# Kernel optimization log

Hardware: AMD Instinct MI355X
Metric: run time of the kernel (lower is better)

The kernel has to match this reference:

```python
import jax, jax.numpy as jnp
import numpy as np

NUM_EXPERTS = 8
IN_FEATURES = 2048
OUT_FEATURES = 5632
GROUP_SIZE = 64
NUM_TOKENS = 4096


def setup_inputs() -> dict:
    key = jax.random.key(0)
    k1, k2, k3, k4 = jax.random.split(key, 4)
    inp = jax.random.normal(k1, (NUM_TOKENS, IN_FEATURES), dtype=jnp.float32)
    # tokens are pre-sorted contiguously per expert; balanced routing
    tokens_per_expert = jnp.full((NUM_EXPERTS,), NUM_TOKENS // NUM_EXPERTS, dtype=jnp.int32)
    # int4 quantized weights stored as integer codes in [0, 16)
    weights = jax.random.randint(k2, (NUM_EXPERTS, IN_FEATURES, OUT_FEATURES), 0, 16, dtype=jnp.int32)
    n_groups = IN_FEATURES // GROUP_SIZE
    scales = jax.random.uniform(k3, (NUM_EXPERTS, n_groups, OUT_FEATURES, 1), dtype=jnp.float32,
                                minval=0.005, maxval=0.02)
    zeros = jax.random.normal(k4, (NUM_EXPERTS, n_groups, OUT_FEATURES, 1), dtype=jnp.float32) * 0.01
    scales_and_zeros = jnp.concatenate([scales, zeros], axis=-1)  # [E, K//G, N, 2]
    return {"input": inp, "tokens_per_expert": tokens_per_expert,
            "weights": weights, "scales_and_zeros": scales_and_zeros}


def _dequant(weights, scales_and_zeros):
    # torchao int4 convention: w = (q - 8) * scale + zero, grouped along K
    E, K, N = weights.shape
    n_groups = scales_and_zeros.shape[1]
    g = K // n_groups
    q = weights.astype(jnp.float32).reshape(E, n_groups, g, N)
    s = scales_and_zeros[..., 0][:, :, None, :]  # [E, K//G, 1, N]
    z = scales_and_zeros[..., 1][:, :, None, :]
    return ((q - 8.0) * s + z).reshape(E, K, N)


def reference(input, tokens_per_expert, weights, scales_and_zeros):
    num_tokens, K = input.shape
    E = weights.shape[0]
    W = _dequant(weights, scales_and_zeros)  # [E, K, N] float32
    # expert id of each (contiguous-sorted) token from cumsum boundaries
    cum = jnp.cumsum(tokens_per_expert)                      # [E]
    seg = jnp.searchsorted(cum, jnp.arange(num_tokens), side='right')  # [T]
    start = jnp.concatenate([jnp.zeros((1,), cum.dtype), cum[:-1]])
    pos = jnp.arange(num_tokens) - start[seg]                # slot within expert block
    # capacity-based grouped GEMM (balanced routing in setup: C = T // E)
    C = num_tokens // E
    buf = jnp.zeros((E, C, K), input.dtype).at[seg, pos].set(input)
    y = jnp.einsum('eck,ekn->ecn', buf, W)                   # per-expert GEMM
    return y[seg, pos]                                       # [T, N]
```

## Files before the change

kernel.cpp:

```cpp
#include <hip/hip_runtime.h>

#define NE    8
#define KDIM  2048
#define NDIM  5632
#define NTOK  4096
#define CAP   512
#define NGRP  32
#define BM    128
#define BN    128
#define BK    32
#define MT    4
#define NT    44
#define LDSS  40

#define K8      (KDIM / 8)
#define NBLK_N  (NDIM / 256)
#define PACK_BLOCKS (NE * K8 * NBLK_N)
#define ACV_BLOCKS  (NTOK * KDIM / (8 * 256))
#define PACKED_BYTES ((size_t)NE * K8 * NDIM * 4)
#define ABF_BYTES    ((size_t)NTOK * KDIM * 2)

typedef __attribute__((ext_vector_type(8))) short bf16x8;
typedef __attribute__((ext_vector_type(4))) short bf16x4;
typedef __attribute__((ext_vector_type(4))) float f32x4;

static __device__ __forceinline__ short f2bf(float f) {
    union { float f; unsigned u; } x; x.f = f;
    unsigned r = (x.u + 0x7fffu + ((x.u >> 16) & 1u)) >> 16;
    return (short)r;
}

__global__ __launch_bounds__(256)
void pack_kernel(const int* __restrict__ wq, const float* __restrict__ inp,
                 unsigned* __restrict__ pw, unsigned short* __restrict__ abf)
{
    const int bid = blockIdx.x;
    if (bid < PACK_BLOCKS) {
        const int e  = bid / (K8 * NBLK_N);
        const int r  = bid % (K8 * NBLK_N);
        const int k8 = r / NBLK_N;
        const int nb = r % NBLK_N;
        const int n  = nb * 256 + threadIdx.x;
        const int* src = wq + ((size_t)e * KDIM + k8 * 8) * NDIM + n;
        unsigned v = 0;
        #pragma unroll
        for (int j = 0; j < 8; ++j)
            v |= (unsigned)(src[(size_t)j * NDIM] & 15) << (4 * j);
        pw[((size_t)e * K8 + k8) * NDIM + n] = v;
    } else {
        const size_t t = (size_t)(bid - PACK_BLOCKS) * 256 + threadIdx.x;
        const float4* p = (const float4*)inp + t * 2;
        const float4 v0 = p[0], v1 = p[1];
        bf16x8 h;
        h[0] = f2bf(v0.x); h[1] = f2bf(v0.y); h[2] = f2bf(v0.z); h[3] = f2bf(v0.w);
        h[4] = f2bf(v1.x); h[5] = f2bf(v1.y); h[6] = f2bf(v1.z); h[7] = f2bf(v1.w);
        *((bf16x8*)abf + t) = h;
    }
}

__global__ __launch_bounds__(256, 2)
void hqq_gemm2(const unsigned short* __restrict__ abf,
               const unsigned*       __restrict__ pw,
               const float*          __restrict__ sz,
               float*                __restrict__ out)
{
    const int bid = blockIdx.x;
    const int e   = bid / (MT * NT);
    const int rem = bid % (MT * NT);
    const int nt  = rem >> 2;
    const int mt  = rem & 3;

    __shared__ __align__(16) short Alds[BM * LDSS];
    __shared__ __align__(16) short Blds[BN * LDSS];

    const int tid = threadIdx.x;
    const int m0  = e * CAP + mt * BM;
    const int n0  = nt * BN;

    const int a_kq  = tid & 3;
    const int a_row = tid >> 2;
    const int b_n   = tid & 127;
    const int b_h   = tid >> 7;

    const unsigned short* Ab = abf + (size_t)m0 * KDIM;
    const unsigned*       Wb = pw  + (size_t)e * K8 * NDIM + n0 + b_n;
    const float*          SZb = sz + (size_t)e * NGRP * (NDIM * 2) + (size_t)(n0 + b_n) * 2;

    f32x4 acc[4][4];
    #pragma unroll
    for (int i = 0; i < 4; ++i)
        #pragma unroll
        for (int j = 0; j < 4; ++j)
            acc[i][j] = (f32x4){0.f, 0.f, 0.f, 0.f};

    const int wave = tid >> 6;
    const int lane = tid & 63;
    const int wm = (wave >> 1) << 6;
    const int wn = (wave & 1) << 6;
    const int lr = lane & 15;
    const int lq = lane >> 4;

    for (int k0 = 0; k0 < KDIM; k0 += BK) {
        const int g = k0 >> 6;

        #pragma unroll
        for (int p = 0; p < 2; ++p) {
            const int row = a_row + p * 64;
            const bf16x8 v = *(const bf16x8*)(Ab + (size_t)row * KDIM + k0 + a_kq * 8);
            *(bf16x8*)&Alds[row * LDSS + a_kq * 8] = v;
        }

        const float2 s2 = *(const float2*)(SZb + (size_t)g * (NDIM * 2));
        const float s  = s2.x;
        const float z8 = s2.y - 8.f * s2.x;
        const unsigned* wp = Wb + ((size_t)(k0 >> 3) + b_h * 2) * NDIM;
        const unsigned u0 = wp[0];
        const unsigned u1 = wp[NDIM];
        bf16x8 bb0, bb1;
        #pragma unroll
        for (int j = 0; j < 8; ++j) {
            bb0[j] = f2bf(fmaf((float)((u0 >> (4 * j)) & 15u), s, z8));
            bb1[j] = f2bf(fmaf((float)((u1 >> (4 * j)) & 15u), s, z8));
        }
        *(bf16x8*)&Blds[b_n * LDSS + b_h * 16]     = bb0;
        *(bf16x8*)&Blds[b_n * LDSS + b_h * 16 + 8] = bb1;

        __syncthreads();

        bf16x8 af[4], bfv[4];
        #pragma unroll
        for (int i = 0; i < 4; ++i)
            af[i] = *(const bf16x8*)&Alds[(wm + i * 16 + lr) * LDSS + lq * 8];
        #pragma unroll
        for (int j = 0; j < 4; ++j)
            bfv[j] = *(const bf16x8*)&Blds[(wn + j * 16 + lr) * LDSS + lq * 8];
        #pragma unroll
        for (int i = 0; i < 4; ++i)
            #pragma unroll
            for (int j = 0; j < 4; ++j)
                acc[i][j] = __builtin_amdgcn_mfma_f32_16x16x32_bf16(af[i], bfv[j], acc[i][j], 0, 0, 0);

        __syncthreads();
    }

    const int orow0 = m0 + wm + lq * 4;
    const int ocol0 = n0 + wn + lr;
    #pragma unroll
    for (int i = 0; i < 4; ++i)
        #pragma unroll
        for (int r = 0; r < 4; ++r) {
            float* op = out + (size_t)(orow0 + i * 16 + r) * NDIM + ocol0;
            #pragma unroll
            for (int j = 0; j < 4; ++j)
                op[j * 16] = acc[i][j][r];
        }
}

__global__ __launch_bounds__(256, 2)
void hqq_gemm_fallback(const float* __restrict__ inp,
                       const int*   __restrict__ wq,
                       const float* __restrict__ sz,
                       float*       __restrict__ out)
{
    const int bid = blockIdx.x;
    const int e   = bid / (MT * NT);
    const int rem = bid % (MT * NT);
    const int nt  = rem >> 2;
    const int mt  = rem & 3;

    __shared__ __align__(16) short Alds[BM * LDSS];
    __shared__ __align__(16) short Blds[BN * LDSS];

    const int tid = threadIdx.x;
    const int m0  = e * CAP + mt * BM;
    const int n0  = nt * BN;

    const int a_kq  = tid & 7;
    const int a_row = tid >> 3;
    const int b_n   = tid & 127;
    const int b_h   = tid >> 7;

    const float* Ab  = inp + (size_t)m0 * KDIM;
    const int*   Wb  = wq  + (size_t)e * KDIM * NDIM + n0 + b_n;
    const float* SZb = sz  + (size_t)e * NGRP * (NDIM * 2) + (size_t)(n0 + b_n) * 2;

    f32x4 acc[4][4];
    #pragma unroll
    for (int i = 0; i < 4; ++i)
        #pragma unroll
        for (int j = 0; j < 4; ++j)
            acc[i][j] = (f32x4){0.f, 0.f, 0.f, 0.f};

    const int wave = tid >> 6;
    const int lane = tid & 63;
    const int wm = (wave >> 1) << 6;
    const int wn = (wave & 1) << 6;
    const int lr = lane & 15;
    const int lq = lane >> 4;

    for (int k0 = 0; k0 < KDIM; k0 += BK) {
        const int g = k0 >> 6;
        #pragma unroll
        for (int p = 0; p < 4; ++p) {
            const int row = a_row + p * 32;
            const float4 v = *(const float4*)(Ab + (size_t)row * KDIM + k0 + a_kq * 4);
            bf16x4 h;
            h[0] = f2bf(v.x); h[1] = f2bf(v.y); h[2] = f2bf(v.z); h[3] = f2bf(v.w);
            *(bf16x4*)&Alds[row * LDSS + a_kq * 4] = h;
        }
        const float2 s2 = *(const float2*)(SZb + (size_t)g * (NDIM * 2));
        const float s  = s2.x;
        const float z8 = s2.y - 8.f * s2.x;
        #pragma unroll
        for (int oo = 0; oo < 2; ++oo) {
            const int ko = b_h * 8 + oo * 16;
            const int* wp = Wb + (size_t)(k0 + ko) * NDIM;
            bf16x8 bb;
            #pragma unroll
            for (int j = 0; j < 8; ++j) {
                const float q = (float)wp[(size_t)j * NDIM];
                bb[j] = f2bf(fmaf(q, s, z8));
            }
            *(bf16x8*)&Blds[b_n * LDSS + ko] = bb;
        }
        __syncthreads();
        bf16x8 af[4], bfv[4];
        #pragma unroll
        for (int i = 0; i < 4; ++i)
            af[i] = *(const bf16x8*)&Alds[(wm + i * 16 + lr) * LDSS + lq * 8];
        #pragma unroll
        for (int j = 0; j < 4; ++j)
            bfv[j] = *(const bf16x8*)&Blds[(wn + j * 16 + lr) * LDSS + lq * 8];
        #pragma unroll
        for (int i = 0; i < 4; ++i)
            #pragma unroll
            for (int j = 0; j < 4; ++j)
                acc[i][j] = __builtin_amdgcn_mfma_f32_16x16x32_bf16(af[i], bfv[j], acc[i][j], 0, 0, 0);
        __syncthreads();
    }

    const int orow0 = m0 + wm + lq * 4;
    const int ocol0 = n0 + wn + lr;
    #pragma unroll
    for (int i = 0; i < 4; ++i)
        #pragma unroll
        for (int r = 0; r < 4; ++r) {
            float* op = out + (size_t)(orow0 + i * 16 + r) * NDIM + ocol0;
            #pragma unroll
            for (int j = 0; j < 4; ++j)
                op[j * 16] = acc[i][j][r];
        }
}

extern "C" void kernel_launch(void* const* d_in, const int* in_sizes, int n_in,
                              void* d_out, int out_size, void* d_ws, size_t ws_size,
                              hipStream_t stream) {
    const float* inp = (const float*)d_in[0];
    const int*   wq  = (const int*)d_in[2];
    const float* sz  = (const float*)d_in[3];
    float*       out = (float*)d_out;

    if (ws_size >= PACKED_BYTES + ABF_BYTES) {
        unsigned*       pw  = (unsigned*)d_ws;
        unsigned short* abf = (unsigned short*)((char*)d_ws + PACKED_BYTES);
        pack_kernel<<<dim3(PACK_BLOCKS + ACV_BLOCKS), dim3(256), 0, stream>>>(wq, inp, pw, abf);
        hqq_gemm2<<<dim3(NE * MT * NT), dim3(256), 0, stream>>>(abf, pw, sz, out);
    } else {
        hqq_gemm_fallback<<<dim3(NE * MT * NT), dim3(256), 0, stream>>>(inp, wq, sz, out);
    }
}
```

Baseline: 674.1 us.

## Predequantize weights to transposed bf16 and stream tiles via global_load_lds

The prep kernel now fully dequantizes the int4 codes into a bf16 weight matrix transposed to [E, N, K], using an LDS transpose, instead of packing nibbles. The GEMM then loads A and B tiles directly into LDS with global_load_lds 16-byte loads, with no in-loop dequant arithmetic and no register staging. The trade is a larger workspace and more prep traffic (bf16 weights are 4x the packed size) for a simpler main loop. The unpadded LDS layout may introduce bank conflicts, and the workspace-size condition may now fail and route to the fallback.

```diff
diff --git a/kernel.cpp b/kernel.cpp
--- a/kernel.cpp
+++ b/kernel.cpp
@@ -11,58 +11,98 @@
 #define BK    32
 #define MT    4
 #define NT    44
-#define LDSS  40
-
-#define K8      (KDIM / 8)
-#define NBLK_N  (NDIM / 256)
-#define PACK_BLOCKS (NE * K8 * NBLK_N)
+
+#define NBT   44
+#define TRB   (NE * NGRP * NBT)
 #define ACV_BLOCKS  (NTOK * KDIM / (8 * 256))
-#define PACKED_BYTES ((size_t)NE * K8 * NDIM * 4)
-#define ABF_BYTES    ((size_t)NTOK * KDIM * 2)
+#define PS    134
+
+#define WT_BYTES  ((size_t)NE * KDIM * NDIM * 2)
+#define ABF_BYTES ((size_t)NTOK * KDIM * 2)
 
 typedef __attribute__((ext_vector_type(8))) short bf16x8;
 typedef __attribute__((ext_vector_type(4))) short bf16x4;
 typedef __attribute__((ext_vector_type(4))) float f32x4;
 
-static __device__ __forceinline__ short f2bf(float f) {
+typedef __attribute__((address_space(3))) unsigned int* lds_p;
+typedef const __attribute__((address_space(1))) unsigned int* glb_p;
+
+static __device__ __forceinline__ void ld16(const void* g, void* l) {
+    __builtin_amdgcn_global_load_lds((glb_p)g, (lds_p)l, 16, 0, 0);
+}
+
+static __device__ __forceinline__ unsigned short f2bf(float f) {
     union { float f; unsigned u; } x; x.f = f;
-    unsigned r = (x.u + 0x7fffu + ((x.u >> 16) & 1u)) >> 16;
-    return (short)r;
+    return (unsigned short)((x.u + 0x7fffu + ((x.u >> 16) & 1u)) >> 16);
 }
 
 __global__ __launch_bounds__(256)
-void pack_kernel(const int* __restrict__ wq, const float* __restrict__ inp,
-                 unsigned* __restrict__ pw, unsigned short* __restrict__ abf)
+void prep_kernel(const int* __restrict__ wq, const float* __restrict__ inp,
+                 const float* __restrict__ sz,
+                 unsigned short* __restrict__ wt, unsigned short* __restrict__ abf)
 {
     const int bid = blockIdx.x;
-    if (bid < PACK_BLOCKS) {
-        const int e  = bid / (K8 * NBLK_N);
-        const int r  = bid % (K8 * NBLK_N);
-        const int k8 = r / NBLK_N;
-        const int nb = r % NBLK_N;
-        const int n  = nb * 256 + threadIdx.x;
-        const int* src = wq + ((size_t)e * KDIM + k8 * 8) * NDIM + n;
-        unsigned v = 0;
-        #pragma unroll
-        for (int j = 0; j < 8; ++j)
-            v |= (unsigned)(src[(size_t)j * NDIM] & 15) << (4 * j);
-        pw[((size_t)e * K8 + k8) * NDIM + n] = v;
+    if (bid < TRB) {
+        const int e  = bid / (NGRP * NBT);
+        const int r  = bid % (NGRP * NBT);
+        const int g  = r / NBT;
+        const int nb = r % NBT;
+        __shared__ unsigned short T[64 * PS];
+        const int t = threadIdx.x;
+
+        const int n4    = (t & 31) * 4;
+        const int r0    = t >> 5;
+        const int nglob = nb * 128 + n4;
+        const float* szp = sz + ((size_t)(e * NGRP + g) * NDIM + nglob) * 2;
+        const float4 sz01 = *(const float4*)szp;
+        const float4 sz23 = *(const float4*)(szp + 4);
+        const float s0 = sz01.x, z0 = sz01.y - 8.f * sz01.x;
+        const float s1 = sz01.z, z1 = sz01.w - 8.f * sz01.z;
+        const float s2 = sz23.x, z2 = sz23.y - 8.f * sz23.x;
+        const float s3 = sz23.z, z3 = sz23.w - 8.f * sz23.z;
+        const int* cbase = wq + (size_t)(e * KDIM + g * 64) * NDIM + nglob;
+        #pragma unroll
+        for (int ri = 0; ri < 8; ++ri) {
+            const int row = r0 + ri * 8;
+            const int4 c = *(const int4*)(cbase + (size_t)row * NDIM);
+            unsigned p0 = (unsigned)f2bf(fmaf((float)c.x, s0, z0))
+                        | ((unsigned)f2bf(fmaf((float)c.y, s1, z1)) << 16);
+            unsigned p1 = (unsigned)f2bf(fmaf((float)c.z, s2, z2))
+                        | ((unsigned)f2bf(fmaf((float)c.w, s3, z3)) << 16);
+            unsigned* dst = (unsigned*)&T[row * PS + n4];
+            dst[0] = p0; dst[1] = p1;
+        }
+        __syncthreads();
+
+        const int kq = t & 7;
+        #pragma unroll
+        for (int it = 0; it < 4; ++it) {
+            const int n = it * 32 + (t >> 3);
+            bf16x8 v;
+            #pragma unroll
+            for (int i = 0; i < 8; ++i)
+                v[i] = (short)T[(kq * 8 + i) * PS + n];
+            unsigned short* dp = wt + ((size_t)e * NDIM + nb * 128 + n) * KDIM
+                                    + g * 64 + kq * 8;
+            *(bf16x8*)dp = v;
+        }
     } else {
-        const size_t t = (size_t)(bid - PACK_BLOCKS) * 256 + threadIdx.x;
+        const size_t t = (size_t)(bid - TRB) * 256 + threadIdx.x;
         const float4* p = (const float4*)inp + t * 2;
         const float4 v0 = p[0], v1 = p[1];
         bf16x8 h;
-        h[0] = f2bf(v0.x); h[1] = f2bf(v0.y); h[2] = f2bf(v0.z); h[3] = f2bf(v0.w);
-        h[4] = f2bf(v1.x); h[5] = f2bf(v1.y); h[6] = f2bf(v1.z); h[7] = f2bf(v1.w);
+        h[0] = (short)f2bf(v0.x); h[1] = (short)f2bf(v0.y);
+        h[2] = (short)f2bf(v0.z); h[3] = (short)f2bf(v0.w);
+        h[4] = (short)f2bf(v1.x); h[5] = (short)f2bf(v1.y);
+        h[6] = (short)f2bf(v1.z); h[7] = (short)f2bf(v1.w);
         *((bf16x8*)abf + t) = h;
     }
 }
 
-__global__ __launch_bounds__(256, 2)
-void hqq_gemm2(const unsigned short* __restrict__ abf,
-               const unsigned*       __restrict__ pw,
-               const float*          __restrict__ sz,
-               float*                __restrict__ out)
+__global__ __launch_bounds__(256)
+void hqq_gemm3(const unsigned short* __restrict__ abf,
+               const unsigned short* __restrict__ wt,
+               float* __restrict__ out)
 {
     const int bid = blockIdx.x;
     const int e   = bid / (MT * NT);
@@ -70,70 +110,53 @@
     const int nt  = rem >> 2;
     const int mt  = rem & 3;
 
-    __shared__ __align__(16) short Alds[BM * LDSS];
-    __shared__ __align__(16) short Blds[BN * LDSS];
-
-    const int tid = threadIdx.x;
-    const int m0  = e * CAP + mt * BM;
-    const int n0  = nt * BN;
-
-    const int a_kq  = tid & 3;
-    const int a_row = tid >> 2;
-    const int b_n   = tid & 127;
-    const int b_h   = tid >> 7;
-
-    const unsigned short* Ab = abf + (size_t)m0 * KDIM;
-    const unsigned*       Wb = pw  + (size_t)e * K8 * NDIM + n0 + b_n;
-    const float*          SZb = sz + (size_t)e * NGRP * (NDIM * 2) + (size_t)(n0 + b_n) * 2;
-
-    f32x4 acc[4][4];
-    #pragma unroll
-    for (int i = 0; i < 4; ++i)
-        #pragma unroll
-        for (int j = 0; j < 4; ++j)
-            acc[i][j] = (f32x4){0.f, 0.f, 0.f, 0.f};
-
+    __shared__ __align__(16) unsigned short Alds[BM * BK];
+    __shared__ __align__(16) unsigned short Blds[BN * BK];
+
+    const int tid  = threadIdx.x;
     const int wave = tid >> 6;
     const int lane = tid & 63;
+    const int m0   = e * CAP + mt * BM;
+    const int n0   = nt * BN;
+
+    const int srow = wave * 32 + (lane >> 2);
+    const int skq  = lane & 3;
+    const unsigned short* Ag0 = abf + (size_t)(m0 + srow) * KDIM + skq * 8;
+    const unsigned short* Ag1 = Ag0 + (size_t)16 * KDIM;
+    const unsigned short* Bg0 = wt + ((size_t)e * NDIM + n0 + srow) * KDIM + skq * 8;
+    const unsigned short* Bg1 = Bg0 + (size_t)16 * KDIM;
+    unsigned short* Al0 = &Alds[wave * 1024];
+    unsigned short* Al1 = &Alds[wave * 1024 + 512];
+    unsigned short* Bl0 = &Blds[wave * 1024];
+    unsigned short* Bl1 = &Blds[wave * 1024 + 512];
+
+    f32x4 acc[4][4];
+    #pragma unroll
+    for (int i = 0; i < 4; ++i)
+        #pragma unroll
+        for (int j = 0; j < 4; ++j)
+            acc[i][j] = (f32x4){0.f, 0.f, 0.f, 0.f};
+
     const int wm = (wave >> 1) << 6;
     const int wn = (wave & 1) << 6;
     const int lr = lane & 15;
     const int lq = lane >> 4;
 
-    for (int k0 = 0; k0 < KDIM; k0 += BK) {
-        const int g = k0 >> 6;
-
-        #pragma unroll
-        for (int p = 0; p < 2; ++p) {
-            const int row = a_row + p * 64;
-            const bf16x8 v = *(const bf16x8*)(Ab + (size_t)row * KDIM + k0 + a_kq * 8);
-            *(bf16x8*)&Alds[row * LDSS + a_kq * 8] = v;
-        }
-
-        const float2 s2 = *(const float2*)(SZb + (size_t)g * (NDIM * 2));
-        const float s  = s2.x;
-        const float z8 = s2.y - 8.f * s2.x;
-        const unsigned* wp = Wb + ((size_t)(k0 >> 3) + b_h * 2) * NDIM;
-        const unsigned u0 = wp[0];
-        const unsigned u1 = wp[NDIM];
-        bf16x8 bb0, bb1;
-        #pragma unroll
-        for (int j = 0; j < 8; ++j) {
-            bb0[j] = f2bf(fmaf((float)((u0 >> (4 * j)) & 15u), s, z8));
-            bb1[j] = f2bf(fmaf((float)((u1 >> (4 * j)) & 15u), s, z8));
-        }
-        *(bf16x8*)&Blds[b_n * LDSS + b_h * 16]     = bb0;
-        *(bf16x8*)&Blds[b_n * LDSS + b_h * 16 + 8] = bb1;
-
+    for (int kk = 0; kk < KDIM / BK; ++kk) {
+        ld16(Ag0, Al0);
+        ld16(Ag1, Al1);
+        ld16(Bg0, Bl0);
+        ld16(Bg1, Bl1);
+        Ag0 += BK; Ag1 += BK; Bg0 += BK; Bg1 += BK;
         __syncthreads();
 
         bf16x8 af[4], bfv[4];
         #pragma unroll
         for (int i = 0; i < 4; ++i)
-            af[i] = *(const bf16x8*)&Alds[(wm + i * 16 + lr) * LDSS + lq * 8];
-        #pragma unroll
-        for (int j = 0; j < 4; ++j)
-            bfv[j] = *(const bf16x8*)&Blds[(wn + j * 16 + lr) * LDSS + lq * 8];
+            af[i] = *(const bf16x8*)&Alds[(wm + i * 16 + lr) * BK + lq * 8];
+        #pragma unroll
+        for (int j = 0; j < 4; ++j)
+            bfv[j] = *(const bf16x8*)&Blds[(wn + j * 16 + lr) * BK + lq * 8];
         #pragma unroll
         for (int i = 0; i < 4; ++i)
             #pragma unroll
@@ -156,6 +179,7 @@
         }
 }
 
+#define LDSS  40
 __global__ __launch_bounds__(256, 2)
 void hqq_gemm_fallback(const float* __restrict__ inp,
                        const int*   __restrict__ wq,
@@ -205,7 +229,8 @@
             const int row = a_row + p * 32;
             const float4 v = *(const float4*)(Ab + (size_t)row * KDIM + k0 + a_kq * 4);
             bf16x4 h;
-            h[0] = f2bf(v.x); h[1] = f2bf(v.y); h[2] = f2bf(v.z); h[3] = f2bf(v.w);
+            h[0] = (short)f2bf(v.x); h[1] = (short)f2bf(v.y);
+            h[2] = (short)f2bf(v.z); h[3] = (short)f2bf(v.w);
             *(bf16x4*)&Alds[row * LDSS + a_kq * 4] = h;
         }
         const float2 s2 = *(const float2*)(SZb + (size_t)g * (NDIM * 2));
@@ -219,7 +244,7 @@
             #pragma unroll
             for (int j = 0; j < 8; ++j) {
                 const float q = (float)wp[(size_t)j * NDIM];
-                bb[j] = f2bf(fmaf(q, s, z8));
+                bb[j] = (short)f2bf(fmaf(q, s, z8));
             }
             *(bf16x8*)&Blds[b_n * LDSS + ko] = bb;
         }
@@ -260,11 +285,11 @@
     const float* sz  = (const float*)d_in[3];
     float*       out = (float*)d_out;
 
-    if (ws_size >= PACKED_BYTES + ABF_BYTES) {
-        unsigned*       pw  = (unsigned*)d_ws;
-        unsigned short* abf = (unsigned short*)((char*)d_ws + PACKED_BYTES);
-        pack_kernel<<<dim3(PACK_BLOCKS + ACV_BLOCKS), dim3(256), 0, stream>>>(wq, inp, pw, abf);
-        hqq_gemm2<<<dim3(NE * MT * NT), dim3(256), 0, stream>>>(abf, pw, sz, out);
+    if (ws_size >= WT_BYTES + ABF_BYTES) {
+        unsigned short* wt  = (unsigned short*)d_ws;
+        unsigned short* abf = (unsigned short*)((char*)d_ws + WT_BYTES);
+        prep_kernel<<<dim3(TRB + ACV_BLOCKS), dim3(256), 0, stream>>>(wq, inp, sz, wt, abf);
+        hqq_gemm3<<<dim3(NE * MT * NT), dim3(256), 0, stream>>>(abf, wt, out);
     } else {
         hqq_gemm_fallback<<<dim3(NE * MT * NT), dim3(256), 0, stream>>>(inp, wq, sz, out);
     }
```

Result: slower. 719.8 us (+6.8%).
